# Kernel optimization log

Hardware: AMD Instinct MI355X
Metric: run time of the kernel (lower is better)

Reference implementation:

```python
import jax, jax.numpy as jnp
import numpy as np

ELEM, EMBD, WIN = 128, 128, 128

def setup_inputs() -> dict:
    key = jax.random.key(0)
    ks = jax.random.split(key, 7)
    s = 1.0 / np.sqrt(ELEM)
    return {
        "x": jax.random.normal(ks[0], (8, 16384, ELEM), dtype=jnp.float32),
        "Wq": jax.random.uniform(ks[1], (EMBD, ELEM), jnp.float32, -s, s),
        "bq": jax.random.uniform(ks[2], (EMBD,), jnp.float32, -s, s),
        "Wk": jax.random.uniform(ks[3], (EMBD, ELEM), jnp.float32, -s, s),
        "bk": jax.random.uniform(ks[4], (EMBD,), jnp.float32, -s, s),
        "Wv": jax.random.uniform(ks[5], (EMBD, ELEM), jnp.float32, -s, s),
        "bv": jax.random.uniform(ks[6], (EMBD,), jnp.float32, -s, s),
    }

def reference(x, Wq, bq, Wk, bk, Wv, bv):
    N, S, E = x.shape
    P = S // WIN
    xp = x.reshape(N, P, WIN, E)  # [N,P,W,E]
    q = jnp.einsum('npwe,de->npwd', xp, Wq) + bq
    k = jnp.einsum('npwe,de->npwd', xp, Wk) + bk
    v = jnp.einsum('npwe,de->npwd', xp, Wv) + bv
    # note: original applies NO 1/sqrt(d) scaling
    scores = jnp.einsum('npwd,npud->npwu', q, k)  # [N,P,W,W]
    attn = jax.nn.softmax(scores, axis=-1)
    out = jnp.einsum('npwu,npud->npwd', attn, v)
    return out.reshape(N, S, EMBD)
```

## Files before the change

### kernel.cpp

```cpp
#include <hip/hip_runtime.h>

#define LDSP 136

typedef _Float16 h8 __attribute__((ext_vector_type(8)));
typedef _Float16 h4 __attribute__((ext_vector_type(4)));
typedef float    f4 __attribute__((ext_vector_type(4)));

__global__ void wconv(const float* __restrict__ Wq, const float* __restrict__ Wk,
                      const float* __restrict__ Wv, _Float16* __restrict__ o) {
    int v = blockIdx.x * 256 + threadIdx.x;
    int arr = v >> 12;
    int off = (v & 4095) * 4;
    const float* s = arr == 0 ? Wq : (arr == 1 ? Wk : Wv);
    f4 f = *(const f4*)(s + off);
    h4 h = {(_Float16)f.x, (_Float16)f.y, (_Float16)f.z, (_Float16)f.w};
    *(h4*)(o + arr * 16384 + off) = h;
}

__global__ __launch_bounds__(512, 2) void attn(
    const float* __restrict__ x, const _Float16* __restrict__ Wb,
    const float* __restrict__ bq, const float* __restrict__ bk,
    const float* __restrict__ bv, float* __restrict__ out) {
    __shared__ _Float16 Xs[128 * LDSP];
    __shared__ _Float16 Qs[128 * LDSP];
    __shared__ _Float16 Ks[128 * LDSP];
    __shared__ _Float16 Vs[128 * LDSP];

    const int tid  = threadIdx.x;
    const int wave = tid >> 6;
    const int lane = tid & 63;
    const int quad = lane >> 4;
    const int l16  = lane & 15;
    const int wb   = wave * 16;
    const size_t base = (size_t)blockIdx.x * (128 * 128);

    const _Float16* Wqb = Wb;
    const _Float16* Wkb = Wb + 16384;
    const _Float16* Wvb = Wb + 32768;

    for (int i = tid; i < 4096; i += 512) {
        int idx = i * 4, row = idx >> 7, col = idx & 127;
        f4 f = *(const f4*)(x + base + idx);
        h4 h = {(_Float16)f.x, (_Float16)f.y, (_Float16)f.z, (_Float16)f.w};
        *(h4*)(&Xs[row * LDSP + col]) = h;
    }
    __syncthreads();

    {
        f4 accQ[8], accK[8], accV[8];
        h8 aQ[4], aK[4], aV[4];
        for (int e0 = 0; e0 < 4; ++e0) {
            aQ[e0] = *(const h8*)(Wqb + (wb + l16) * 128 + e0 * 32 + quad * 8);
            aK[e0] = *(const h8*)(Wkb + (wb + l16) * 128 + e0 * 32 + quad * 8);
            aV[e0] = *(const h8*)(Wvb + (wb + l16) * 128 + e0 * 32 + quad * 8);
        }
        f4 bq4 = *(const f4*)(bq + wb + quad * 4);
        f4 bk4 = *(const f4*)(bk + wb + quad * 4);
        float bvv = bv[wb + l16];
        for (int t = 0; t < 8; ++t) {
            accQ[t] = bq4;
            accK[t] = bk4;
            accV[t] = (f4){bvv, bvv, bvv, bvv};
        }
        for (int e0 = 0; e0 < 4; ++e0) {
            h8 b[8];
            for (int nt = 0; nt < 8; ++nt)
                b[nt] = *(const h8*)(&Xs[(nt * 16 + l16) * LDSP + e0 * 32 + quad * 8]);
            for (int nt = 0; nt < 8; ++nt) {
                accQ[nt] = __builtin_amdgcn_mfma_f32_16x16x32_f16(aQ[e0], b[nt], accQ[nt], 0, 0, 0);
                accK[nt] = __builtin_amdgcn_mfma_f32_16x16x32_f16(aK[e0], b[nt], accK[nt], 0, 0, 0);
                accV[nt] = __builtin_amdgcn_mfma_f32_16x16x32_f16(b[nt], aV[e0], accV[nt], 0, 0, 0);
            }
        }
        for (int nt = 0; nt < 8; ++nt) {
            f4 v = accQ[nt];
            h4 h = {(_Float16)v.x, (_Float16)v.y, (_Float16)v.z, (_Float16)v.w};
            *(h4*)(&Qs[(nt * 16 + l16) * LDSP + wb + quad * 4]) = h;
            v = accK[nt];
            h4 g = {(_Float16)v.x, (_Float16)v.y, (_Float16)v.z, (_Float16)v.w};
            *(h4*)(&Ks[(nt * 16 + l16) * LDSP + wb + quad * 4]) = g;
        }
        for (int mt = 0; mt < 8; ++mt) {
            f4 v = accV[mt];
            h4 h = {(_Float16)v.x, (_Float16)v.y, (_Float16)v.z, (_Float16)v.w};
            *(h4*)(&Vs[(wb + l16) * LDSP + mt * 16 + quad * 4]) = h;
        }
    }
    __syncthreads();

    f4 acc[8];
    for (int mt = 0; mt < 8; ++mt) acc[mt] = (f4){0.f, 0.f, 0.f, 0.f};
    for (int d0 = 0; d0 < 4; ++d0) {
        h8 bqf = *(const h8*)(&Qs[(wb + l16) * LDSP + d0 * 32 + quad * 8]);
        h8 a[8];
        for (int mt = 0; mt < 8; ++mt)
            a[mt] = *(const h8*)(&Ks[(mt * 16 + l16) * LDSP + d0 * 32 + quad * 8]);
        for (int mt = 0; mt < 8; ++mt)
            acc[mt] = __builtin_amdgcn_mfma_f32_16x16x32_f16(a[mt], bqf, acc[mt], 0, 0, 0);
    }
    {
        float m = -1e30f;
        for (int mt = 0; mt < 8; ++mt) {
            f4 v = acc[mt];
            m = fmaxf(m, fmaxf(fmaxf(v.x, v.y), fmaxf(v.z, v.w)));
        }
        m = fmaxf(m, __shfl_xor(m, 16, 64));
        m = fmaxf(m, __shfl_xor(m, 32, 64));
        float s = 0.f;
        for (int mt = 0; mt < 8; ++mt) {
            f4 v = acc[mt];
            v.x = __expf(v.x - m); v.y = __expf(v.y - m);
            v.z = __expf(v.z - m); v.w = __expf(v.w - m);
            acc[mt] = v;
            s += v.x + v.y + v.z + v.w;
        }
        s += __shfl_xor(s, 16, 64);
        s += __shfl_xor(s, 32, 64);
        float inv = 1.0f / s;
        _Float16* Ps = Xs;
        for (int mt = 0; mt < 8; ++mt) {
            f4 v = acc[mt];
            h4 h = {(_Float16)(v.x * inv), (_Float16)(v.y * inv),
                    (_Float16)(v.z * inv), (_Float16)(v.w * inv)};
            *(h4*)(&Ps[(wb + l16) * LDSP + mt * 16 + quad * 4]) = h;
        }
    }

    for (int nt = 0; nt < 8; ++nt) acc[nt] = (f4){0.f, 0.f, 0.f, 0.f};
    for (int u0 = 0; u0 < 4; ++u0) {
        h8 ap = *(const h8*)(&Xs[(wb + l16) * LDSP + u0 * 32 + quad * 8]);
        h8 b[8];
        for (int nt = 0; nt < 8; ++nt)
            b[nt] = *(const h8*)(&Vs[(nt * 16 + l16) * LDSP + u0 * 32 + quad * 8]);
        for (int nt = 0; nt < 8; ++nt)
            acc[nt] = __builtin_amdgcn_mfma_f32_16x16x32_f16(ap, b[nt], acc[nt], 0, 0, 0);
    }
    float* ob = out + base;
    for (int nt = 0; nt < 8; ++nt) {
        f4 v = acc[nt];
        int w0 = wb + quad * 4;
        int d  = nt * 16 + l16;
        ob[(size_t)(w0 + 0) * 128 + d] = v.x;
        ob[(size_t)(w0 + 1) * 128 + d] = v.y;
        ob[(size_t)(w0 + 2) * 128 + d] = v.z;
        ob[(size_t)(w0 + 3) * 128 + d] = v.w;
    }
}

extern "C" void kernel_launch(void* const* d_in, const int* in_sizes, int n_in,
                              void* d_out, int out_size, void* d_ws, size_t ws_size,
                              hipStream_t stream) {
    const float* x  = (const float*)d_in[0];
    const float* Wq = (const float*)d_in[1];
    const float* bq = (const float*)d_in[2];
    const float* Wk = (const float*)d_in[3];
    const float* bk = (const float*)d_in[4];
    const float* Wv = (const float*)d_in[5];
    const float* bv = (const float*)d_in[6];
    _Float16* Wb = (_Float16*)d_ws;

    wconv<<<48, 256, 0, stream>>>(Wq, Wk, Wv, Wb);
    attn<<<1024, 512, 0, stream>>>(x, Wb, bq, bk, bv, (float*)d_out);
}
```

Before: 151.0 us.

## Fold Wq·Wk into one matrix and loop four windows per block with prefetch

Precomputes M = Wq^T·Wk and the bias term bq·Wk on the device, so each window needs two projections (T = x·M and V) instead of three. Scores become x·T^T plus a per-key bias. The bk terms are dropped because they only shift each softmax row by a constant. The attention kernel becomes persistent: 256 blocks each handle four windows, with the next window's x prefetched into registers while the current one is computed. This trades fewer MFMAs and better latency hiding for the risk of extra fp16 rounding in the fused M matrix and two small serial prep kernels.

```diff
diff --git a/kernel.cpp b/kernel.cpp
--- a/kernel.cpp
+++ b/kernel.cpp
@@ -6,24 +6,39 @@
 typedef _Float16 h4 __attribute__((ext_vector_type(4)));
 typedef float    f4 __attribute__((ext_vector_type(4)));
 
-__global__ void wconv(const float* __restrict__ Wq, const float* __restrict__ Wk,
-                      const float* __restrict__ Wv, _Float16* __restrict__ o) {
-    int v = blockIdx.x * 256 + threadIdx.x;
-    int arr = v >> 12;
-    int off = (v & 4095) * 4;
-    const float* s = arr == 0 ? Wq : (arr == 1 ? Wk : Wv);
-    f4 f = *(const f4*)(s + off);
-    h4 h = {(_Float16)f.x, (_Float16)f.y, (_Float16)f.z, (_Float16)f.w};
-    *(h4*)(o + arr * 16384 + off) = h;
+__global__ void prep_mt(const float* __restrict__ Wq, const float* __restrict__ Wk,
+                        _Float16* __restrict__ Mt) {
+    int idx = blockIdx.x * 256 + threadIdx.x;
+    int e = idx & 127, f = idx >> 7;
+    float acc = 0.f;
+    for (int d = 0; d < 128; ++d)
+        acc += Wk[d * 128 + f] * Wq[d * 128 + e];
+    Mt[idx] = (_Float16)acc;
+}
+
+__global__ void prep_rest(const float* __restrict__ Wv, const float* __restrict__ Wk,
+                          const float* __restrict__ bq, _Float16* __restrict__ Wvh,
+                          float* __restrict__ ck) {
+    int t = threadIdx.x;
+    for (int i = 0; i < 16; ++i) {
+        int off = (t + i * 256) * 4;
+        f4 f = *(const f4*)(Wv + off);
+        h4 h = {(_Float16)f.x, (_Float16)f.y, (_Float16)f.z, (_Float16)f.w};
+        *(h4*)(Wvh + off) = h;
+    }
+    if (t < 128) {
+        float acc = 0.f;
+        for (int d = 0; d < 128; ++d) acc += bq[d] * Wk[d * 128 + t];
+        ck[t] = acc;
+    }
 }
 
 __global__ __launch_bounds__(512, 2) void attn(
-    const float* __restrict__ x, const _Float16* __restrict__ Wb,
-    const float* __restrict__ bq, const float* __restrict__ bk,
+    const float* __restrict__ x, const _Float16* __restrict__ Mt,
+    const _Float16* __restrict__ Wvh, const float* __restrict__ ck,
     const float* __restrict__ bv, float* __restrict__ out) {
-    __shared__ _Float16 Xs[128 * LDSP];
-    __shared__ _Float16 Qs[128 * LDSP];
-    __shared__ _Float16 Ks[128 * LDSP];
+    __shared__ _Float16 Xs[2][128 * LDSP];
+    __shared__ _Float16 Ts[128 * LDSP];
     __shared__ _Float16 Vs[128 * LDSP];
 
     const int tid  = threadIdx.x;
@@ -32,118 +47,121 @@
     const int quad = lane >> 4;
     const int l16  = lane & 15;
     const int wb   = wave * 16;
-    const size_t base = (size_t)blockIdx.x * (128 * 128);
 
-    const _Float16* Wqb = Wb;
-    const _Float16* Wkb = Wb + 16384;
-    const _Float16* Wvb = Wb + 32768;
+    h8 aT[4], aV[4];
+    for (int e0 = 0; e0 < 4; ++e0) {
+        aT[e0] = *(const h8*)(Mt  + (wb + l16) * 128 + e0 * 32 + quad * 8);
+        aV[e0] = *(const h8*)(Wvh + (wb + l16) * 128 + e0 * 32 + quad * 8);
+    }
+    f4 ck4  = *(const f4*)(ck + wb + quad * 4);
+    float bvv = bv[wb + l16];
 
-    for (int i = tid; i < 4096; i += 512) {
-        int idx = i * 4, row = idx >> 7, col = idx & 127;
-        f4 f = *(const f4*)(x + base + idx);
-        h4 h = {(_Float16)f.x, (_Float16)f.y, (_Float16)f.z, (_Float16)f.w};
-        *(h4*)(&Xs[row * LDSP + col]) = h;
-    }
-    __syncthreads();
+    const size_t base0 = (size_t)blockIdx.x * 4 * (128 * 128);
 
-    {
-        f4 accQ[8], accK[8], accV[8];
-        h8 aQ[4], aK[4], aV[4];
-        for (int e0 = 0; e0 < 4; ++e0) {
-            aQ[e0] = *(const h8*)(Wqb + (wb + l16) * 128 + e0 * 32 + quad * 8);
-            aK[e0] = *(const h8*)(Wkb + (wb + l16) * 128 + e0 * 32 + quad * 8);
-            aV[e0] = *(const h8*)(Wvb + (wb + l16) * 128 + e0 * 32 + quad * 8);
+    f4 pf[8];
+    for (int j = 0; j < 8; ++j)
+        pf[j] = *(const f4*)(x + base0 + 4 * tid + 2048 * j);
+
+    for (int it = 0; it < 4; ++it) {
+        _Float16* X = Xs[it & 1];
+
+        for (int j = 0; j < 8; ++j) {
+            int idx = 4 * tid + 2048 * j;
+            int row = idx >> 7, col = idx & 127;
+            f4 f = pf[j];
+            h4 h = {(_Float16)f.x, (_Float16)f.y, (_Float16)f.z, (_Float16)f.w};
+            *(h4*)(&X[row * LDSP + col]) = h;
         }
-        f4 bq4 = *(const f4*)(bq + wb + quad * 4);
-        f4 bk4 = *(const f4*)(bk + wb + quad * 4);
-        float bvv = bv[wb + l16];
-        for (int t = 0; t < 8; ++t) {
-            accQ[t] = bq4;
-            accK[t] = bk4;
-            accV[t] = (f4){bvv, bvv, bvv, bvv};
+        __syncthreads();
+
+        if (it < 3) {
+            const float* nx = x + base0 + (size_t)(it + 1) * (128 * 128);
+            for (int j = 0; j < 8; ++j)
+                pf[j] = *(const f4*)(nx + 4 * tid + 2048 * j);
         }
-        for (int e0 = 0; e0 < 4; ++e0) {
+
+        {
+            f4 accT[8], accV[8];
+            for (int t = 0; t < 8; ++t) {
+                accT[t] = ck4;
+                accV[t] = (f4){bvv, bvv, bvv, bvv};
+            }
+            for (int e0 = 0; e0 < 4; ++e0) {
+                h8 b[8];
+                for (int nt = 0; nt < 8; ++nt)
+                    b[nt] = *(const h8*)(&X[(nt * 16 + l16) * LDSP + e0 * 32 + quad * 8]);
+                for (int nt = 0; nt < 8; ++nt) {
+                    accT[nt] = __builtin_amdgcn_mfma_f32_16x16x32_f16(aT[e0], b[nt], accT[nt], 0, 0, 0);
+                    accV[nt] = __builtin_amdgcn_mfma_f32_16x16x32_f16(b[nt], aV[e0], accV[nt], 0, 0, 0);
+                }
+            }
+            for (int nt = 0; nt < 8; ++nt) {
+                f4 v = accT[nt];
+                h4 h = {(_Float16)v.x, (_Float16)v.y, (_Float16)v.z, (_Float16)v.w};
+                *(h4*)(&Ts[(nt * 16 + l16) * LDSP + wb + quad * 4]) = h;
+                v = accV[nt];
+                h4 g = {(_Float16)v.x, (_Float16)v.y, (_Float16)v.z, (_Float16)v.w};
+                *(h4*)(&Vs[(wb + l16) * LDSP + nt * 16 + quad * 4]) = g;
+            }
+        }
+        __syncthreads();
+
+        f4 acc[8];
+        for (int mt = 0; mt < 8; ++mt) acc[mt] = (f4){0.f, 0.f, 0.f, 0.f};
+        for (int f0 = 0; f0 < 4; ++f0) {
+            h8 bt = *(const h8*)(&Ts[(wb + l16) * LDSP + f0 * 32 + quad * 8]);
+            h8 a[8];
+            for (int mt = 0; mt < 8; ++mt)
+                a[mt] = *(const h8*)(&X[(mt * 16 + l16) * LDSP + f0 * 32 + quad * 8]);
+            for (int mt = 0; mt < 8; ++mt)
+                acc[mt] = __builtin_amdgcn_mfma_f32_16x16x32_f16(a[mt], bt, acc[mt], 0, 0, 0);
+        }
+        {
+            float m = -1e30f;
+            for (int mt = 0; mt < 8; ++mt) {
+                f4 v = acc[mt];
+                m = fmaxf(m, fmaxf(fmaxf(v.x, v.y), fmaxf(v.z, v.w)));
+            }
+            m = fmaxf(m, __shfl_xor(m, 16, 64));
+            m = fmaxf(m, __shfl_xor(m, 32, 64));
+            float s = 0.f;
+            for (int mt = 0; mt < 8; ++mt) {
+                f4 v = acc[mt];
+                v.x = __expf(v.x - m); v.y = __expf(v.y - m);
+                v.z = __expf(v.z - m); v.w = __expf(v.w - m);
+                acc[mt] = v;
+                s += v.x + v.y + v.z + v.w;
+            }
+            s += __shfl_xor(s, 16, 64);
+            s += __shfl_xor(s, 32, 64);
+            float inv = 1.0f / s;
+            for (int mt = 0; mt < 8; ++mt) {
+                f4 v = acc[mt];
+                h4 h = {(_Float16)(v.x * inv), (_Float16)(v.y * inv),
+                        (_Float16)(v.z * inv), (_Float16)(v.w * inv)};
+                *(h4*)(&Ts[(wb + l16) * LDSP + mt * 16 + quad * 4]) = h;
+            }
+        }
+
+        for (int nt = 0; nt < 8; ++nt) acc[nt] = (f4){0.f, 0.f, 0.f, 0.f};
+        for (int u0 = 0; u0 < 4; ++u0) {
+            h8 ap = *(const h8*)(&Ts[(wb + l16) * LDSP + u0 * 32 + quad * 8]);
             h8 b[8];
             for (int nt = 0; nt < 8; ++nt)
-                b[nt] = *(const h8*)(&Xs[(nt * 16 + l16) * LDSP + e0 * 32 + quad * 8]);
-            for (int nt = 0; nt < 8; ++nt) {
-                accQ[nt] = __builtin_amdgcn_mfma_f32_16x16x32_f16(aQ[e0], b[nt], accQ[nt], 0, 0, 0);
-                accK[nt] = __builtin_amdgcn_mfma_f32_16x16x32_f16(aK[e0], b[nt], accK[nt], 0, 0, 0);
-                accV[nt] = __builtin_amdgcn_mfma_f32_16x16x32_f16(b[nt], aV[e0], accV[nt], 0, 0, 0);
-            }
+                b[nt] = *(const h8*)(&Vs[(nt * 16 + l16) * LDSP + u0 * 32 + quad * 8]);
+            for (int nt = 0; nt < 8; ++nt)
+                acc[nt] = __builtin_amdgcn_mfma_f32_16x16x32_f16(ap, b[nt], acc[nt], 0, 0, 0);
         }
+        float* ob = out + base0 + (size_t)it * (128 * 128);
         for (int nt = 0; nt < 8; ++nt) {
-            f4 v = accQ[nt];
-            h4 h = {(_Float16)v.x, (_Float16)v.y, (_Float16)v.z, (_Float16)v.w};
-            *(h4*)(&Qs[(nt * 16 + l16) * LDSP + wb + quad * 4]) = h;
-            v = accK[nt];
-            h4 g = {(_Float16)v.x, (_Float16)v.y, (_Float16)v.z, (_Float16)v.w};
-            *(h4*)(&Ks[(nt * 16 + l16) * LDSP + wb + quad * 4]) = g;
+            f4 v = acc[nt];
+            int w0 = wb + quad * 4;
+            int d  = nt * 16 + l16;
+            ob[(size_t)(w0 + 0) * 128 + d] = v.x;
+            ob[(size_t)(w0 + 1) * 128 + d] = v.y;
+            ob[(size_t)(w0 + 2) * 128 + d] = v.z;
+            ob[(size_t)(w0 + 3) * 128 + d] = v.w;
         }
-        for (int mt = 0; mt < 8; ++mt) {
-            f4 v = accV[mt];
-            h4 h = {(_Float16)v.x, (_Float16)v.y, (_Float16)v.z, (_Float16)v.w};
-            *(h4*)(&Vs[(wb + l16) * LDSP + mt * 16 + quad * 4]) = h;
-        }
-    }
-    __syncthreads();
-
-    f4 acc[8];
-    for (int mt = 0; mt < 8; ++mt) acc[mt] = (f4){0.f, 0.f, 0.f, 0.f};
-    for (int d0 = 0; d0 < 4; ++d0) {
-        h8 bqf = *(const h8*)(&Qs[(wb + l16) * LDSP + d0 * 32 + quad * 8]);
-        h8 a[8];
-        for (int mt = 0; mt < 8; ++mt)
-            a[mt] = *(const h8*)(&Ks[(mt * 16 + l16) * LDSP + d0 * 32 + quad * 8]);
-        for (int mt = 0; mt < 8; ++mt)
-            acc[mt] = __builtin_amdgcn_mfma_f32_16x16x32_f16(a[mt], bqf, acc[mt], 0, 0, 0);
-    }
-    {
-        float m = -1e30f;
-        for (int mt = 0; mt < 8; ++mt) {
-            f4 v = acc[mt];
-            m = fmaxf(m, fmaxf(fmaxf(v.x, v.y), fmaxf(v.z, v.w)));
-        }
-        m = fmaxf(m, __shfl_xor(m, 16, 64));
-        m = fmaxf(m, __shfl_xor(m, 32, 64));
-        float s = 0.f;
-        for (int mt = 0; mt < 8; ++mt) {
-            f4 v = acc[mt];
-            v.x = __expf(v.x - m); v.y = __expf(v.y - m);
-            v.z = __expf(v.z - m); v.w = __expf(v.w - m);
-            acc[mt] = v;
-            s += v.x + v.y + v.z + v.w;
-        }
-        s += __shfl_xor(s, 16, 64);
-        s += __shfl_xor(s, 32, 64);
-        float inv = 1.0f / s;
-        _Float16* Ps = Xs;
-        for (int mt = 0; mt < 8; ++mt) {
-            f4 v = acc[mt];
-            h4 h = {(_Float16)(v.x * inv), (_Float16)(v.y * inv),
-                    (_Float16)(v.z * inv), (_Float16)(v.w * inv)};
-            *(h4*)(&Ps[(wb + l16) * LDSP + mt * 16 + quad * 4]) = h;
-        }
-    }
-
-    for (int nt = 0; nt < 8; ++nt) acc[nt] = (f4){0.f, 0.f, 0.f, 0.f};
-    for (int u0 = 0; u0 < 4; ++u0) {
-        h8 ap = *(const h8*)(&Xs[(wb + l16) * LDSP + u0 * 32 + quad * 8]);
-        h8 b[8];
-        for (int nt = 0; nt < 8; ++nt)
-            b[nt] = *(const h8*)(&Vs[(nt * 16 + l16) * LDSP + u0 * 32 + quad * 8]);
-        for (int nt = 0; nt < 8; ++nt)
-            acc[nt] = __builtin_amdgcn_mfma_f32_16x16x32_f16(ap, b[nt], acc[nt], 0, 0, 0);
-    }
-    float* ob = out + base;
-    for (int nt = 0; nt < 8; ++nt) {
-        f4 v = acc[nt];
-        int w0 = wb + quad * 4;
-        int d  = nt * 16 + l16;
-        ob[(size_t)(w0 + 0) * 128 + d] = v.x;
-        ob[(size_t)(w0 + 1) * 128 + d] = v.y;
-        ob[(size_t)(w0 + 2) * 128 + d] = v.z;
-        ob[(size_t)(w0 + 3) * 128 + d] = v.w;
     }
 }
 
@@ -154,11 +172,14 @@
     const float* Wq = (const float*)d_in[1];
     const float* bq = (const float*)d_in[2];
     const float* Wk = (const float*)d_in[3];
-    const float* bk = (const float*)d_in[4];
     const float* Wv = (const float*)d_in[5];
     const float* bv = (const float*)d_in[6];
-    _Float16* Wb = (_Float16*)d_ws;
 
-    wconv<<<48, 256, 0, stream>>>(Wq, Wk, Wv, Wb);
-    attn<<<1024, 512, 0, stream>>>(x, Wb, bq, bk, bv, (float*)d_out);
+    _Float16* Mt  = (_Float16*)d_ws;
+    _Float16* Wvh = Mt + 16384;
+    float*    ckp = (float*)(Wvh + 16384);
+
+    prep_mt<<<64, 256, 0, stream>>>(Wq, Wk, Mt);
+    prep_rest<<<1, 256, 0, stream>>>(Wv, Wk, bq, Wvh, ckp);
+    attn<<<256, 512, 0, stream>>>(x, Mt, Wvh, ckp, bv, (float*)d_out);
 }
```

Result: faster. 142.5 us (-5.6%).
